# Optimization experiments

Measured on AMD Instinct MI355X. Metric: run time of the kernel, lower is better.

## Reference

```python
import jax, jax.numpy as jnp
import numpy as np
import math

B, S, DIM = 2, 2048, 2048
H, KV = 32, 8
HD = DIM // H          # 64
REP = H // KV          # 4
NEG = -1e9


def setup_inputs() -> dict:
    key = jax.random.key(0)
    ks = jax.random.split(key, 8)
    x = jax.random.normal(ks[0], (B, S, DIM), dtype=jnp.float32)
    # RoPE frequencies: theta = 10000^{-2i/d}, angles = pos * theta
    inv_freq = 1.0 / (10000.0 ** (jnp.arange(0, HD, 2, dtype=jnp.float32) / HD))  # [HD/2]
    angles = jnp.arange(S, dtype=jnp.float32)[:, None] * inv_freq[None, :]        # [S, HD/2]
    freqs_cos = jnp.cos(angles)
    freqs_sin = jnp.sin(angles)
    # additive causal mask [1,1,S,S]
    causal = jnp.tril(jnp.ones((S, S), dtype=bool))
    mask = jnp.where(causal, 0.0, NEG).astype(jnp.float32)[None, None]
    sc = 1.0 / math.sqrt(DIM)
    wq = jax.random.normal(ks[1], (DIM, H * HD), dtype=jnp.float32) * sc
    wk = jax.random.normal(ks[2], (DIM, KV * HD), dtype=jnp.float32) * sc
    wv = jax.random.normal(ks[3], (DIM, KV * HD), dtype=jnp.float32) * sc
    wo = jax.random.normal(ks[4], (H * HD, DIM), dtype=jnp.float32) * sc
    return {"x": x, "freqs_cos": freqs_cos, "freqs_sin": freqs_sin,
            "mask": mask, "wq": wq, "wk": wk, "wv": wv, "wo": wo}


def _rope(t, cos, sin):
    # t: [B,S,nh,HD]; interleaved (even, odd) pairs == view_as_complex layout
    te, to = t[..., 0::2], t[..., 1::2]
    c = cos[None, :, None, :]  # [1,S,1,HD/2]
    s = sin[None, :, None, :]
    oe = te * c - to * s
    oo = te * s + to * c
    return jnp.stack([oe, oo], axis=-1).reshape(t.shape)


def reference(x, freqs_cos, freqs_sin, mask, wq, wk, wv, wo):
    b, s, _ = x.shape
    q = (x @ wq).reshape(b, s, H, HD)
    k = (x @ wk).reshape(b, s, KV, HD)
    v = (x @ wv).reshape(b, s, KV, HD)
    q = _rope(q, freqs_cos, freqs_sin)
    k = _rope(k, freqs_cos, freqs_sin)
    # GQA without materializing repeat_interleave: group q heads by kv head
    # repeat_interleave maps query head h -> kv head h // REP
    qg = q.transpose(0, 2, 1, 3).reshape(b, KV, REP, s, HD)  # [B,KV,REP,S,HD]
    kg = k.transpose(0, 2, 1, 3)                              # [B,KV,S,HD]
    vg = v.transpose(0, 2, 1, 3)
    scores = jnp.einsum('bgrqd,bgkd->bgrqk', qg, kg) / math.sqrt(HD)
    scores = scores + mask[:, :, None]                        # [1,1,1,S,S] broadcast
    attn = jax.nn.softmax(scores, axis=-1)
    out = jnp.einsum('bgrqk,bgkd->bgrqd', attn, vg)           # [B,KV,REP,S,HD]
    out = out.reshape(b, H, s, HD).transpose(0, 2, 1, 3).reshape(b, s, H * HD)
    return out @ wo
```

## Files before the change

kernel.cpp:

```cpp
#include <hip/hip_runtime.h>
#include <hip/hip_bf16.h>

#define B_ 2
#define S_ 2048
#define DIM_ 2048
#define H_ 32
#define KV_ 8
#define HD_ 64

typedef __bf16 bf16x8 __attribute__((ext_vector_type(8)));
typedef __bf16 bf16x4 __attribute__((ext_vector_type(4)));
typedef float f32x4 __attribute__((ext_vector_type(4)));
typedef float f32x16 __attribute__((ext_vector_type(16)));
typedef unsigned u32x2 __attribute__((ext_vector_type(2)));

#define GLOAD16(gp, lp) __builtin_amdgcn_global_load_lds( \
    (const __attribute__((address_space(1))) void*)(gp),  \
    (__attribute__((address_space(3))) void*)(lp), 16, 0, 0)

__global__ __launch_bounds__(256) void cast_f32_bf16_v4(const float* __restrict__ in,
                                                        __bf16* __restrict__ out, int n4) {
    int i = blockIdx.x * 256 + threadIdx.x;
    if (i >= n4) return;
    float4 v = ((const float4*)in)[i];
    bf16x4 o;
    o[0] = (__bf16)v.x; o[1] = (__bf16)v.y; o[2] = (__bf16)v.z; o[3] = (__bf16)v.w;
    ((bf16x4*)out)[i] = o;
}

__global__ __launch_bounds__(256) void transpose_all_t(const float* __restrict__ wq,
                                                       const float* __restrict__ wk,
                                                       const float* __restrict__ wv,
                                                       const float* __restrict__ wo,
                                                       __bf16* __restrict__ wqkv_t,
                                                       __bf16* __restrict__ wo_t) {
    __shared__ float t[32][33];
    const int bk = blockIdx.x * 32, bn = blockIdx.y * 32;
    const int tx = threadIdx.x & 31, ty = threadIdx.x >> 5;
    const float* W; __bf16* Wt; int N, src;
    if (blockIdx.z == 0) {
        Wt = wqkv_t;
        if (bn < 2048)      { W = wq; N = 2048; src = bn; }
        else if (bn < 2560) { W = wk; N = 512;  src = bn - 2048; }
        else                { W = wv; N = 512;  src = bn - 2560; }
    } else {
        if (bn >= 2048) return;
        Wt = wo_t; W = wo; N = 2048; src = bn;
    }
#pragma unroll
    for (int i = 0; i < 4; i++)
        t[ty * 4 + i][tx] = W[(size_t)(bk + ty * 4 + i) * N + src + tx];
    __syncthreads();
#pragma unroll
    for (int i = 0; i < 4; i++)
        Wt[(size_t)(bn + ty * 4 + i) * 2048 + bk + tx] = (__bf16)t[tx][ty * 4 + i];
}

__global__ __launch_bounds__(512, 4)
void gemm256_qkv(const __bf16* __restrict__ A, const __bf16* __restrict__ Bt,
                 __bf16* __restrict__ q_bf, __bf16* __restrict__ k_bf,
                 __bf16* __restrict__ vt_bf,
                 const float* __restrict__ fc, const float* __restrict__ fs) {
    __shared__ __align__(16) char smem[81920];
    char* lA = smem;
    char* lB = smem + 32768;
    const int K = DIM_;
    const int tid = threadIdx.x, lane = tid & 63, wid = tid >> 6;
    const int wr2 = wid >> 2, wc2 = wid & 3;
    const int fr = lane & 15, fg = lane >> 4;
    const int id = blockIdx.x;
    const long i0 = (long)(id >> 4) * 128;
    const long j0 = (long)(id & 15) * 192;

    const int r0 = tid >> 3;
    const int cc = ((tid & 7) ^ (r0 & 7)) * 8;
    const __bf16* pA = A + (i0 + r0) * (long)K + cc;
    const __bf16* pB = Bt + (j0 + r0) * (long)K + cc;
    const int NT = K >> 6;

    f32x4 acc[4][3] = {};

#define STG(kt, buf) do { \
    GLOAD16(pA + (long)(kt) * 64,                  lA + (buf) * 16384 + tid * 16); \
    GLOAD16(pA + (long)64 * K + (long)(kt) * 64,   lA + (buf) * 16384 + 8192 + tid * 16); \
    GLOAD16(pB + (long)(kt) * 64,                  lB + (buf) * 24576 + tid * 16); \
    GLOAD16(pB + (long)64 * K + (long)(kt) * 64,   lB + (buf) * 24576 + 8192 + tid * 16); \
    GLOAD16(pB + (long)128 * K + (long)(kt) * 64,  lB + (buf) * 24576 + 16384 + tid * 16); } while (0)

    STG(0, 0);

    for (int kt = 0; kt < NT; ++kt) {
        const int cur = kt & 1, nxt = cur ^ 1;
        const bool nl = (kt + 1 < NT);
        const char* cA = lA + cur * 16384;
        const char* cB = lB + cur * 24576;

        if (nl) STG(kt + 1, nxt);
        if (nl) asm volatile("s_waitcnt vmcnt(5)" ::: "memory");
        else    asm volatile("s_waitcnt vmcnt(0)" ::: "memory");
        __builtin_amdgcn_s_barrier();
        asm volatile("" ::: "memory");

        bf16x8 af[4], bfv[3];
#pragma unroll
        for (int ks = 0; ks < 2; ks++) {
#pragma unroll
            for (int nf = 0; nf < 3; nf++) {
                int row = wc2 * 48 + nf * 16 + fr;
                bfv[nf] = *(const bf16x8*)(cB + row * 128 + (((ks << 2) | fg) ^ (row & 7)) * 16);
            }
#pragma unroll
            for (int mf = 0; mf < 4; mf++) {
                int row = wr2 * 64 + mf * 16 + fr;
                af[mf] = *(const bf16x8*)(cA + row * 128 + (((ks << 2) | fg) ^ (row & 7)) * 16);
            }
            __builtin_amdgcn_s_setprio(1);
#pragma unroll
            for (int mf = 0; mf < 4; mf++)
#pragma unroll
                for (int nf = 0; nf < 3; nf++)
                    acc[mf][nf] = __builtin_amdgcn_mfma_f32_16x16x32_bf16(af[mf], bfv[nf], acc[mf][nf], 0, 0, 0);
            __builtin_amdgcn_s_setprio(0);
        }
        __builtin_amdgcn_s_barrier();
    }
#undef STG

#pragma unroll
    for (int mf = 0; mf < 4; mf++)
#pragma unroll
        for (int nf = 0; nf < 3; nf++) {
            const long colf = j0 + wc2 * 48 + nf * 16;
            const long col = colf + fr;
            const long row0 = i0 + wr2 * 64 + mf * 16 + fg * 4;
            if (colf < 2048) {
#pragma unroll
                for (int j = 0; j < 4; j++)
                    q_bf[(row0 + j) * 2048 + col] = (__bf16)acc[mf][nf][j];
            } else if (colf < 2560) {
                const int kd = (int)(col - 2048);
                const int i_ = (kd & 63) >> 1;
                const float sgn = (fr & 1) ? 1.0f : -1.0f;
#pragma unroll
                for (int j = 0; j < 4; j++) {
                    long row = row0 + j;
                    int s = (int)(row & (S_ - 1));
                    float cv = fc[s * 32 + i_], sv = fs[s * 32 + i_];
                    float v = acc[mf][nf][j];
                    float p = __shfl_xor(v, 1, 64);
                    k_bf[row * 512 + kd] = (__bf16)(v * cv + sgn * sv * p);
                }
            } else {
                const int vd = (int)(col - 2560);
                int b = (int)(row0 >> 11);
                int s = (int)(row0 & (S_ - 1));
                bf16x4 pk;
#pragma unroll
                for (int j = 0; j < 4; j++) pk[j] = (__bf16)acc[mf][nf][j];
                *(bf16x4*)(vt_bf + ((size_t)(b * KV_ + (vd >> 6)) * HD_ + (vd & 63)) * S_ + s) = pk;
            }
        }
}

__global__ __launch_bounds__(512, 2)
void gemm256_o(const __bf16* __restrict__ A, const __bf16* __restrict__ Bt,
               float* __restrict__ C) {
    __shared__ __align__(16) char smem[98304];
    char* lA = smem;
    char* lB = smem + 32768;
    const int K = DIM_;
    const int tid = threadIdx.x, lane = tid & 63, wid = tid >> 6;
    const int wr2 = wid >> 2, wc2 = wid & 3;
    const int fr = lane & 15, fg = lane >> 4;
    const int id = blockIdx.x;
    const long i0 = (long)(id >> 3) * 128;
    const long j0 = (long)(id & 7) * 256;

    const int r0 = tid >> 3;
    const int cc = ((tid & 7) ^ (r0 & 7)) * 8;
    const __bf16* pA = A + (i0 + r0) * (long)K + cc;
    const __bf16* pB = Bt + (j0 + r0) * (long)K + cc;
    const int NT = K >> 6;

    f32x4 acc[4][4] = {};

#define STG(kt, buf) do { \
    GLOAD16(pA + (long)(kt) * 64,                  lA + (buf) * 16384 + tid * 16); \
    GLOAD16(pA + (long)64 * K + (long)(kt) * 64,   lA + (buf) * 16384 + 8192 + tid * 16); \
    GLOAD16(pB + (long)(kt) * 64,                  lB + (buf) * 32768 + tid * 16); \
    GLOAD16(pB + (long)64 * K + (long)(kt) * 64,   lB + (buf) * 32768 + 8192 + tid * 16); \
    GLOAD16(pB + (long)128 * K + (long)(kt) * 64,  lB + (buf) * 32768 + 16384 + tid * 16); \
    GLOAD16(pB + (long)192 * K + (long)(kt) * 64,  lB + (buf) * 32768 + 24576 + tid * 16); } while (0)

    STG(0, 0);

    for (int kt = 0; kt < NT; ++kt) {
        const int cur = kt & 1, nxt = cur ^ 1;
        const bool nl = (kt + 1 < NT);
        const char* cA = lA + cur * 16384;
        const char* cB = lB + cur * 32768;

        if (nl) STG(kt + 1, nxt);
        if (nl) asm volatile("s_waitcnt vmcnt(6)" ::: "memory");
        else    asm volatile("s_waitcnt vmcnt(0)" ::: "memory");
        __builtin_amdgcn_s_barrier();
        asm volatile("" ::: "memory");

        bf16x8 af[4], bfv[4];
#pragma unroll
        for (int ks = 0; ks < 2; ks++) {
#pragma unroll
            for (int nf = 0; nf < 4; nf++) {
                int row = wc2 * 64 + nf * 16 + fr;
                bfv[nf] = *(const bf16x8*)(cB + row * 128 + (((ks << 2) | fg) ^ (row & 7)) * 16);
            }
#pragma unroll
            for (int mf = 0; mf < 4; mf++) {
                int row = wr2 * 64 + mf * 16 + fr;
                af[mf] = *(const bf16x8*)(cA + row * 128 + (((ks << 2) | fg) ^ (row & 7)) * 16);
            }
            __builtin_amdgcn_s_setprio(1);
#pragma unroll
            for (int mf = 0; mf < 4; mf++)
#pragma unroll
                for (int nf = 0; nf < 4; nf++)
                    acc[mf][nf] = __builtin_amdgcn_mfma_f32_16x16x32_bf16(af[mf], bfv[nf], acc[mf][nf], 0, 0, 0);
            __builtin_amdgcn_s_setprio(0);
        }
        __builtin_amdgcn_s_barrier();
    }
#undef STG

#pragma unroll
    for (int mf = 0; mf < 4; mf++)
#pragma unroll
        for (int nf = 0; nf < 4; nf++)
#pragma unroll
            for (int j = 0; j < 4; j++) {
                long row = i0 + wr2 * 64 + mf * 16 + fg * 4 + j;
                long col = j0 + wc2 * 64 + nf * 16 + fr;
                C[row * 2048 + col] = acc[mf][nf][j];
            }
}

__global__ __launch_bounds__(256, 4)
void attn_fwd(const __bf16* __restrict__ Q, const __bf16* __restrict__ Kb,
              const __bf16* __restrict__ Vt, __bf16* __restrict__ O,
              const float* __restrict__ fc, const float* __restrict__ fs) {
    extern __shared__ __align__(16) char smem[];
    __bf16* lK  = (__bf16*)smem;
    __bf16* lVt = (__bf16*)(smem + 16384);

    const int tid = threadIdx.x;
    const int lane = tid & 63;
    const int wid = tid >> 6;
    const int ln = lane & 31;
    const int hi = lane >> 5;

    const int id = blockIdx.x;
    const int round = id >> 8;
    const int q4 = (id >> 6) & 3;
    const int inner = id & 63;
    const int g = inner & 7;
    const int hb = inner >> 3;
    const int b = hb & 1;
    const int h = g * 4 + (hb >> 1);
    const int chunk = (round == 0) ? 12 + q4
                    : (round == 1) ? 3 - q4
                    : (round == 2) ? 8 + q4
                    :                7 - q4;
    const int QS = H_ * HD_, KS = KV_ * HD_;
    const float K2 = 0.18033688011112042f;
    const float mK = 8.0f * K2;

    const __bf16* Kbse = Kb + (size_t)(b * S_) * KS + g * HD_;
    const __bf16* Vbse = Vt + (size_t)((b * KV_ + g) * HD_) * S_;

    bf16x8 onesf;
#pragma unroll
    for (int j = 0; j < 8; j++) onesf[j] = (__bf16)1.0f;

    const int c0 = tid, c1 = tid + 256;
    const int kr0 = c0 & 63, kd0 = c0 >> 6;
    const int kr1 = c1 & 63, kd1 = c1 >> 6;
    const __bf16* Ksrc0 = Kbse + (size_t)kr0 * KS + kd0 * 8;
    const __bf16* Ksrc1 = Kbse + (size_t)kr1 * KS + kd1 * 8;
    const __bf16* Vsrc0 = Vbse + (size_t)kr0 * S_ + kd0 * 8;
    const __bf16* Vsrc1 = Vbse + (size_t)kr1 * S_ + kd1 * 8;

    auto stage = [&](int t, int buf) {
        GLOAD16(Ksrc0 + (size_t)t * 64 * KS, lK + buf * 4096 + c0 * 8);
        GLOAD16(Ksrc1 + (size_t)t * 64 * KS, lK + buf * 4096 + c1 * 8);
        GLOAD16(Vsrc0 + t * 64,              lVt + buf * 4096 + c0 * 8);
        GLOAD16(Vsrc1 + t * 64,              lVt + buf * 4096 + c1 * 8);
    };

    const int q0w = chunk * 128 + wid * 32;
    const int qrow = q0w + ln;
    const int nt = 2 * chunk + 2;
    const int nkv_w = (q0w >> 6) + 1;

    const __bf16* Qb = Q + (size_t)(b * S_ + qrow) * QS + h * HD_;
    const float* cz = fc + (size_t)qrow * 32;
    const float* sz = fs + (size_t)qrow * 32;
    bf16x8 qf[4];
#pragma unroll
    for (int kk = 0; kk < 4; kk++) {
        bf16x8 raw = *(const bf16x8*)(Qb + kk * 16 + hi * 8);
#pragma unroll
        for (int p = 0; p < 4; p++) {
            const int i = kk * 8 + hi * 4 + p;
            float cv = cz[i], sv = sz[i];
            float e = (float)raw[2 * p], o = (float)raw[2 * p + 1];
            qf[kk][2 * p]     = (__bf16)(e * cv - o * sv);
            qf[kk][2 * p + 1] = (__bf16)(e * sv + o * cv);
        }
    }

    f32x16 o0 = {}, o1 = {}, o2 = {};

    stage(0, 0);

    for (int t = 0; t < nt; t++) {
        if (t + 1 < nt) {
            stage(t + 1, (t + 1) & 1);
            asm volatile("s_waitcnt vmcnt(4)" ::: "memory");
        } else {
            asm volatile("s_waitcnt vmcnt(0)" ::: "memory");
        }
        __builtin_amdgcn_s_barrier();
        asm volatile("" ::: "memory");
        if (t < nkv_w) {
            const char* lKc = (const char*)(lK + (t & 1) * 4096);
            const char* lVc = (const char*)(lVt + (t & 1) * 4096);
            const int p0 = t * 64;

            f32x16 s0 = {}, s1 = {};
            __builtin_amdgcn_s_setprio(1);
#pragma unroll
            for (int kk = 0; kk < 4; kk++) {
                bf16x8 ka = *(const bf16x8*)(lKc + (kk * 2 + hi) * 1024 + ln * 16);
                s0 = __builtin_amdgcn_mfma_f32_32x32x16_bf16(ka, qf[kk], s0, 0, 0, 0);
            }
#pragma unroll
            for (int kk = 0; kk < 4; kk++) {
                bf16x8 ka = *(const bf16x8*)(lKc + (kk * 2 + hi) * 1024 + (32 + ln) * 16);
                s1 = __builtin_amdgcn_mfma_f32_32x32x16_bf16(ka, qf[kk], s1, 0, 0, 0);
            }
            __builtin_amdgcn_s_setprio(0);

            if (t == nkv_w - 1) {
#pragma unroll
                for (int rr = 0; rr < 16; rr++) {
                    int crow = (rr & 3) + 8 * (rr >> 2) + 4 * hi;
                    if (p0 + crow > qrow)      s0[rr] = -1e30f;
                    if (p0 + 32 + crow > qrow) s1[rr] = -1e30f;
                }
            }

#pragma unroll
            for (int rr = 0; rr < 16; rr++) {
                s0[rr] = exp2f(s0[rr] * K2 - mK);
                s1[rr] = exp2f(s1[rr] * K2 - mK);
            }

            __builtin_amdgcn_s_setprio(1);
#pragma unroll
            for (int c = 0; c < 2; c++) {
                const f32x16& pe = c ? s1 : s0;
                unsigned w[4][2];
#pragma unroll
                for (int gi = 0; gi < 4; gi++)
#pragma unroll
                    for (int p = 0; p < 2; p++) {
                        unsigned short lo = __builtin_bit_cast(unsigned short, (__bf16)pe[4 * gi + 2 * p]);
                        unsigned short hp = __builtin_bit_cast(unsigned short, (__bf16)pe[4 * gi + 2 * p + 1]);
                        w[gi][p] = (unsigned)lo | ((unsigned)hp << 16);
                    }
                unsigned pw0[4], pw1[4];
#pragma unroll
                for (int p = 0; p < 2; p++) {
                    u32x2 ra = __builtin_amdgcn_permlane32_swap(w[0][p], w[1][p], false, false);
                    pw0[p] = ra[0]; pw0[2 + p] = ra[1];
                    u32x2 rb = __builtin_amdgcn_permlane32_swap(w[2][p], w[3][p], false, false);
                    pw1[p] = rb[0]; pw1[2 + p] = rb[1];
                }
                bf16x8 pa0 = __builtin_bit_cast(bf16x8, *(uint4*)pw0);
                bf16x8 pa1 = __builtin_bit_cast(bf16x8, *(uint4*)pw1);
#pragma unroll
                for (int half = 0; half < 2; half++) {
                    const int ks = 2 * c + half;
                    bf16x8 pa = half ? pa1 : pa0;
                    bf16x8 va0 = *(const bf16x8*)(lVc + (ks * 2 + hi) * 1024 + ln * 16);
                    bf16x8 va1 = *(const bf16x8*)(lVc + (ks * 2 + hi) * 1024 + (32 + ln) * 16);
                    o0 = __builtin_amdgcn_mfma_f32_32x32x16_bf16(va0, pa, o0, 0, 0, 0);
                    o1 = __builtin_amdgcn_mfma_f32_32x32x16_bf16(va1, pa, o1, 0, 0, 0);
                    o2 = __builtin_amdgcn_mfma_f32_32x32x16_bf16(onesf, pa, o2, 0, 0, 0);
                }
            }
            __builtin_amdgcn_s_setprio(0);
        }
        __builtin_amdgcn_s_barrier();
    }

    const float inv = 1.0f / o2[0];
    __bf16* Oq = O + (size_t)(b * S_ + qrow) * QS + h * HD_;
#pragma unroll
    for (int db = 0; db < 2; db++) {
        const f32x16& oo = db ? o1 : o0;
#pragma unroll
        for (int gi = 0; gi < 4; gi++) {
            bf16x4 pk;
#pragma unroll
            for (int j = 0; j < 4; j++) pk[j] = (__bf16)(oo[4 * gi + j] * inv);
            *(bf16x4*)(Oq + db * 32 + 8 * gi + 4 * hi) = pk;
        }
    }
}

extern "C" void kernel_launch(void* const* d_in, const int* in_sizes, int n_in,
                              void* d_out, int out_size, void* d_ws, size_t ws_size,
                              hipStream_t stream) {
    const float* x  = (const float*)d_in[0];
    const float* fc = (const float*)d_in[1];
    const float* fs = (const float*)d_in[2];
    const float* wq = (const float*)d_in[4];
    const float* wk = (const float*)d_in[5];
    const float* wv = (const float*)d_in[6];
    const float* wo = (const float*)d_in[7];
    float* out = (float*)d_out;

    const size_t N0 = (size_t)B_ * S_ * DIM_;
    const size_t N1 = (size_t)B_ * S_ * H_ * HD_;
    const size_t N2 = (size_t)B_ * S_ * KV_ * HD_;
    const size_t N3 = (size_t)DIM_ * H_ * HD_;
    const size_t N4 = (size_t)DIM_ * KV_ * HD_;

    __bf16* x_bf = (__bf16*)d_ws;
    __bf16* q_bf = x_bf + N0;
    __bf16* k_bf = q_bf + N1;
    __bf16* vt_bf = k_bf + N2;
    __bf16* wqkv_t = vt_bf + N2;
    __bf16* wo_t = wqkv_t + N3 + 2 * N4;
    __bf16* ao_bf = x_bf;

    cast_f32_bf16_v4<<<dim3(N0 / 4 / 256), 256, 0, stream>>>(x, x_bf, (int)(N0 / 4));
    transpose_all_t<<<dim3(64, 96, 2), 256, 0, stream>>>(wq, wk, wv, wo, wqkv_t, wo_t);

    gemm256_qkv<<<dim3(512), 512, 0, stream>>>(x_bf, wqkv_t, q_bf, k_bf, vt_bf, fc, fs);

    attn_fwd<<<dim3(1024), 256, 32768, stream>>>(q_bf, k_bf, vt_bf, ao_bf, fc, fs);

    gemm256_o<<<dim3(256), 512, 0, stream>>>(ao_bf, wo_t, out);
}
```

Before: 188.8 us.

## Triple-buffer K/V tiles and software-pipeline QK^T one tile ahead of softmax·V

The attention kernel moves from double to triple LDS buffering, loading K/V tiles two iterations ahead. Each step now issues the QK^T MFMAs for tile t+1 before the exp and PV work for tile t, using two ping-pong score register sets so matrix ops can overlap the transcendental work. This raises shared memory to 48KB and lowers the occupancy bound from 4 to 3 blocks per CU, and the extra live score registers add register pressure.

```diff
diff --git a/kernel.cpp b/kernel.cpp
--- a/kernel.cpp
+++ b/kernel.cpp
@@ -243,13 +243,13 @@
             }
 }
 
-__global__ __launch_bounds__(256, 4)
+__global__ __launch_bounds__(256, 3)
 void attn_fwd(const __bf16* __restrict__ Q, const __bf16* __restrict__ Kb,
               const __bf16* __restrict__ Vt, __bf16* __restrict__ O,
               const float* __restrict__ fc, const float* __restrict__ fs) {
     extern __shared__ __align__(16) char smem[];
     __bf16* lK  = (__bf16*)smem;
-    __bf16* lVt = (__bf16*)(smem + 16384);
+    __bf16* lVt = (__bf16*)(smem + 24576);
 
     const int tid = threadIdx.x;
     const int lane = tid & 63;
@@ -288,7 +288,8 @@
     const __bf16* Vsrc0 = Vbse + (size_t)kr0 * S_ + kd0 * 8;
     const __bf16* Vsrc1 = Vbse + (size_t)kr1 * S_ + kd1 * 8;
 
-    auto stage = [&](int t, int buf) {
+    auto stage = [&](int t) {
+        const int buf = t % 3;
         GLOAD16(Ksrc0 + (size_t)t * 64 * KS, lK + buf * 4096 + c0 * 8);
         GLOAD16(Ksrc1 + (size_t)t * 64 * KS, lK + buf * 4096 + c1 * 8);
         GLOAD16(Vsrc0 + t * 64,              lVt + buf * 4096 + c0 * 8);
@@ -318,89 +319,103 @@
     }
 
     f32x16 o0 = {}, o1 = {}, o2 = {};
-
-    stage(0, 0);
-
-    for (int t = 0; t < nt; t++) {
-        if (t + 1 < nt) {
-            stage(t + 1, (t + 1) & 1);
+    f32x16 sA0, sA1, sB0, sB1;
+
+    auto qk_phase = [&](int tt, f32x16& S0, f32x16& S1) {
+        const char* lKc = (const char*)(lK + (tt % 3) * 4096);
+        f32x16 t0 = {}, t1 = {};
+        __builtin_amdgcn_s_setprio(1);
+#pragma unroll
+        for (int kk = 0; kk < 4; kk++) {
+            bf16x8 ka = *(const bf16x8*)(lKc + (kk * 2 + hi) * 1024 + ln * 16);
+            t0 = __builtin_amdgcn_mfma_f32_32x32x16_bf16(ka, qf[kk], t0, 0, 0, 0);
+        }
+#pragma unroll
+        for (int kk = 0; kk < 4; kk++) {
+            bf16x8 ka = *(const bf16x8*)(lKc + (kk * 2 + hi) * 1024 + (32 + ln) * 16);
+            t1 = __builtin_amdgcn_mfma_f32_32x32x16_bf16(ka, qf[kk], t1, 0, 0, 0);
+        }
+        __builtin_amdgcn_s_setprio(0);
+        S0 = t0; S1 = t1;
+    };
+
+    auto smpv_phase = [&](int tt, f32x16& S0, f32x16& S1) {
+        const char* lVc = (const char*)(lVt + (tt % 3) * 4096);
+        const int p0 = tt * 64;
+        if (tt == nkv_w - 1) {
+#pragma unroll
+            for (int rr = 0; rr < 16; rr++) {
+                int crow = (rr & 3) + 8 * (rr >> 2) + 4 * hi;
+                if (p0 + crow > qrow)      S0[rr] = -1e30f;
+                if (p0 + 32 + crow > qrow) S1[rr] = -1e30f;
+            }
+        }
+#pragma unroll
+        for (int rr = 0; rr < 16; rr++) {
+            S0[rr] = exp2f(S0[rr] * K2 - mK);
+            S1[rr] = exp2f(S1[rr] * K2 - mK);
+        }
+        __builtin_amdgcn_s_setprio(1);
+#pragma unroll
+        for (int c = 0; c < 2; c++) {
+            const f32x16& pe = c ? S1 : S0;
+            unsigned w[4][2];
+#pragma unroll
+            for (int gi = 0; gi < 4; gi++)
+#pragma unroll
+                for (int p = 0; p < 2; p++) {
+                    unsigned short lo = __builtin_bit_cast(unsigned short, (__bf16)pe[4 * gi + 2 * p]);
+                    unsigned short hp = __builtin_bit_cast(unsigned short, (__bf16)pe[4 * gi + 2 * p + 1]);
+                    w[gi][p] = (unsigned)lo | ((unsigned)hp << 16);
+                }
+            unsigned pw0[4], pw1[4];
+#pragma unroll
+            for (int p = 0; p < 2; p++) {
+                u32x2 ra = __builtin_amdgcn_permlane32_swap(w[0][p], w[1][p], false, false);
+                pw0[p] = ra[0]; pw0[2 + p] = ra[1];
+                u32x2 rb = __builtin_amdgcn_permlane32_swap(w[2][p], w[3][p], false, false);
+                pw1[p] = rb[0]; pw1[2 + p] = rb[1];
+            }
+            bf16x8 pa0 = __builtin_bit_cast(bf16x8, *(uint4*)pw0);
+            bf16x8 pa1 = __builtin_bit_cast(bf16x8, *(uint4*)pw1);
+#pragma unroll
+            for (int half = 0; half < 2; half++) {
+                const int ks = 2 * c + half;
+                bf16x8 pa = half ? pa1 : pa0;
+                bf16x8 va0 = *(const bf16x8*)(lVc + (ks * 2 + hi) * 1024 + ln * 16);
+                bf16x8 va1 = *(const bf16x8*)(lVc + (ks * 2 + hi) * 1024 + (32 + ln) * 16);
+                o0 = __builtin_amdgcn_mfma_f32_32x32x16_bf16(va0, pa, o0, 0, 0, 0);
+                o1 = __builtin_amdgcn_mfma_f32_32x32x16_bf16(va1, pa, o1, 0, 0, 0);
+                o2 = __builtin_amdgcn_mfma_f32_32x32x16_bf16(onesf, pa, o2, 0, 0, 0);
+            }
+        }
+        __builtin_amdgcn_s_setprio(0);
+    };
+
+    auto step = [&](int t, f32x16& C0, f32x16& C1, f32x16& N0_, f32x16& N1_) {
+        if (t + 2 < nt) {
+            stage(t + 2);
             asm volatile("s_waitcnt vmcnt(4)" ::: "memory");
-        } else {
+        } else if (t + 1 < nt) {
             asm volatile("s_waitcnt vmcnt(0)" ::: "memory");
         }
         __builtin_amdgcn_s_barrier();
         asm volatile("" ::: "memory");
-        if (t < nkv_w) {
-            const char* lKc = (const char*)(lK + (t & 1) * 4096);
-            const char* lVc = (const char*)(lVt + (t & 1) * 4096);
-            const int p0 = t * 64;
-
-            f32x16 s0 = {}, s1 = {};
-            __builtin_amdgcn_s_setprio(1);
-#pragma unroll
-            for (int kk = 0; kk < 4; kk++) {
-                bf16x8 ka = *(const bf16x8*)(lKc + (kk * 2 + hi) * 1024 + ln * 16);
-                s0 = __builtin_amdgcn_mfma_f32_32x32x16_bf16(ka, qf[kk], s0, 0, 0, 0);
-            }
-#pragma unroll
-            for (int kk = 0; kk < 4; kk++) {
-                bf16x8 ka = *(const bf16x8*)(lKc + (kk * 2 + hi) * 1024 + (32 + ln) * 16);
-                s1 = __builtin_amdgcn_mfma_f32_32x32x16_bf16(ka, qf[kk], s1, 0, 0, 0);
-            }
-            __builtin_amdgcn_s_setprio(0);
-
-            if (t == nkv_w - 1) {
-#pragma unroll
-                for (int rr = 0; rr < 16; rr++) {
-                    int crow = (rr & 3) + 8 * (rr >> 2) + 4 * hi;
-                    if (p0 + crow > qrow)      s0[rr] = -1e30f;
-                    if (p0 + 32 + crow > qrow) s1[rr] = -1e30f;
-                }
-            }
-
-#pragma unroll
-            for (int rr = 0; rr < 16; rr++) {
-                s0[rr] = exp2f(s0[rr] * K2 - mK);
-                s1[rr] = exp2f(s1[rr] * K2 - mK);
-            }
-
-            __builtin_amdgcn_s_setprio(1);
-#pragma unroll
-            for (int c = 0; c < 2; c++) {
-                const f32x16& pe = c ? s1 : s0;
-                unsigned w[4][2];
-#pragma unroll
-                for (int gi = 0; gi < 4; gi++)
-#pragma unroll
-                    for (int p = 0; p < 2; p++) {
-                        unsigned short lo = __builtin_bit_cast(unsigned short, (__bf16)pe[4 * gi + 2 * p]);
-                        unsigned short hp = __builtin_bit_cast(unsigned short, (__bf16)pe[4 * gi + 2 * p + 1]);
-                        w[gi][p] = (unsigned)lo | ((unsigned)hp << 16);
-                    }
-                unsigned pw0[4], pw1[4];
-#pragma unroll
-                for (int p = 0; p < 2; p++) {
-                    u32x2 ra = __builtin_amdgcn_permlane32_swap(w[0][p], w[1][p], false, false);
-                    pw0[p] = ra[0]; pw0[2 + p] = ra[1];
-                    u32x2 rb = __builtin_amdgcn_permlane32_swap(w[2][p], w[3][p], false, false);
-                    pw1[p] = rb[0]; pw1[2 + p] = rb[1];
-                }
-                bf16x8 pa0 = __builtin_bit_cast(bf16x8, *(uint4*)pw0);
-                bf16x8 pa1 = __builtin_bit_cast(bf16x8, *(uint4*)pw1);
-#pragma unroll
-                for (int half = 0; half < 2; half++) {
-                    const int ks = 2 * c + half;
-                    bf16x8 pa = half ? pa1 : pa0;
-                    bf16x8 va0 = *(const bf16x8*)(lVc + (ks * 2 + hi) * 1024 + ln * 16);
-                    bf16x8 va1 = *(const bf16x8*)(lVc + (ks * 2 + hi) * 1024 + (32 + ln) * 16);
-                    o0 = __builtin_amdgcn_mfma_f32_32x32x16_bf16(va0, pa, o0, 0, 0, 0);
-                    o1 = __builtin_amdgcn_mfma_f32_32x32x16_bf16(va1, pa, o1, 0, 0, 0);
-                    o2 = __builtin_amdgcn_mfma_f32_32x32x16_bf16(onesf, pa, o2, 0, 0, 0);
-                }
-            }
-            __builtin_amdgcn_s_setprio(0);
-        }
-        __builtin_amdgcn_s_barrier();
+        if (t + 1 < nkv_w) qk_phase(t + 1, N0_, N1_);
+        if (t < nkv_w) smpv_phase(t, C0, C1);
+        __builtin_amdgcn_s_barrier();
+    };
+
+    stage(0);
+    stage(1);
+    asm volatile("s_waitcnt vmcnt(4)" ::: "memory");
+    __builtin_amdgcn_s_barrier();
+    asm volatile("" ::: "memory");
+    qk_phase(0, sA0, sA1);
+
+    for (int t = 0; t < nt; t += 2) {
+        step(t,     sA0, sA1, sB0, sB1);
+        step(t + 1, sB0, sB1, sA0, sA1);
     }
 
     const float inv = 1.0f / o2[0];
@@ -449,7 +464,7 @@
 
     gemm256_qkv<<<dim3(512), 512, 0, stream>>>(x_bf, wqkv_t, q_bf, k_bf, vt_bf, fc, fs);
 
-    attn_fwd<<<dim3(1024), 256, 32768, stream>>>(q_bf, k_bf, vt_bf, ao_bf, fc, fs);
+    attn_fwd<<<dim3(1024), 256, 49152, stream>>>(q_bf, k_bf, vt_bf, ao_bf, fc, fs);
 
     gemm256_o<<<dim3(256), 512, 0, stream>>>(ao_bf, wo_t, out);
 }
```

Result: slower. 196.3 us (+3.9%).
